# Kernel optimization log

Hardware: AMD Instinct MI355X
Metric: run time of the kernel (lower is better)

## Reference

```python
import jax, jax.numpy as jnp
import numpy as np

B, T, C, H = 4, 2048, 1024, 16
D = C // H  # head_dim = 64


def setup_inputs() -> dict:
    key = jax.random.key(0)
    k1, k2, k3, k4, k5 = jax.random.split(key, 5)
    x = jax.random.normal(k1, (B, T, C), dtype=jnp.float32)
    # torch nn.Linear weights: [out_features, in_features]
    s = 1.0 / np.sqrt(C)
    qkv_w = jax.random.uniform(k2, (3 * C, C), dtype=jnp.float32, minval=-s, maxval=s)
    qkv_b = jax.random.uniform(k3, (3 * C,), dtype=jnp.float32, minval=-s, maxval=s)
    out_w = jax.random.uniform(k4, (C, C), dtype=jnp.float32, minval=-s, maxval=s)
    out_b = jax.random.uniform(k5, (C,), dtype=jnp.float32, minval=-s, maxval=s)
    # causal mask broadcastable to [B,H,T,T]; 0 (False) marks masked positions
    attn_mask = jnp.tril(jnp.ones((T, T), dtype=bool))[None, None]
    return {"x": x, "qkv_w": qkv_w, "qkv_b": qkv_b, "out_w": out_w,
            "out_b": out_b, "attn_mask": attn_mask}


def reference(x, qkv_w, qkv_b, out_w, out_b, attn_mask):
    qkv = x @ qkv_w.T + qkv_b                      # [B,T,3C]
    q, k, v = jnp.split(qkv, 3, axis=-1)
    # [B,T,C] -> [B,H,T,D]
    q = q.reshape(B, T, H, D).transpose(0, 2, 1, 3)
    k = k.reshape(B, T, H, D).transpose(0, 2, 1, 3)
    v = v.reshape(B, T, H, D).transpose(0, 2, 1, 3)
    scale = 1.0 / np.sqrt(D)
    attn = jnp.einsum('bhqd,bhkd->bhqk', q, k) * scale   # [B,H,T,T]
    neg = jnp.finfo(attn.dtype).min
    attn = jnp.where(attn_mask, attn, neg)
    attn = jax.nn.softmax(attn, axis=-1)
    out = jnp.einsum('bhqk,bhkd->bhqd', attn, v)          # [B,H,T,D]
    out = out.transpose(0, 2, 1, 3).reshape(B, T, C)
    return out @ out_w.T + out_b
```

## Files before the change

kernel.cpp:

```cpp
#include <hip/hip_runtime.h>
#include <hip/hip_bf16.h>

#define B_ 4
#define T_ 2048
#define C_ 1024
#define H_ 16
#define D_ 64

typedef __hip_bfloat16 bf16;
typedef float f32x4 __attribute__((ext_vector_type(4)));
typedef short bf16s8 __attribute__((ext_vector_type(8)));

#define NEG_BIG (-1e30f)

__device__ inline unsigned short f2bf(float f) {
  __hip_bfloat16 h = __float2bfloat16(f);
  return *reinterpret_cast<unsigned short*>(&h);
}
__device__ inline float bf_lo(unsigned u) {
  union { unsigned u; float f; } c; c.u = u << 16; return c.f;
}

__device__ inline void async_load16(const void* g, void* l) {
  __builtin_amdgcn_global_load_lds(
      (const __attribute__((address_space(1))) unsigned int*)g,
      (__attribute__((address_space(3))) unsigned int*)l, 16, 0, 0);
}

__device__ inline void plswap32(unsigned& a, unsigned& b) {
  auto r = __builtin_amdgcn_permlane32_swap(a, b, false, false);
  a = r[0]; b = r[1];
}
__device__ inline void plswap16(unsigned& a, unsigned& b) {
  auto r = __builtin_amdgcn_permlane16_swap(a, b, false, false);
  a = r[0]; b = r[1];
}

union U4 { uint4 u; unsigned short s[8]; };

__device__ inline uint4 load8(const void* base, size_t idx, int f32) {
  if (f32) {
    const float* p = (const float*)base + idx;
    float4 a = *(const float4*)p;
    float4 b = *(const float4*)(p + 4);
    U4 r;
    r.s[0] = f2bf(a.x); r.s[1] = f2bf(a.y); r.s[2] = f2bf(a.z); r.s[3] = f2bf(a.w);
    r.s[4] = f2bf(b.x); r.s[5] = f2bf(b.y); r.s[6] = f2bf(b.z); r.s[7] = f2bf(b.w);
    return r.u;
  }
  return *(const uint4*)((const unsigned short*)base + idx);
}

__global__ void detect_k(const unsigned short* __restrict__ w, int* __restrict__ flag) {
  int lane = threadIdx.x;
  bool big = false;
  for (int i = lane; i < 512; i += 64) {
    float f = bf_lo((unsigned)w[i]);
    if (!(fabsf(f) <= 1.0f)) big = true;
  }
  int any = __any(big);
  if (lane == 0) *flag = any ? 1 : 0;
}

#define R_X   1048576
#define R_WQ  (R_X + 393216)
#define R_WO  (R_WQ + 131072)
#define R_BQ  (R_WO + 384)
#define R_BO  (R_BQ + 128)
__global__ __launch_bounds__(256) void convert_all_k(
    const void* __restrict__ x, const void* __restrict__ wq,
    const void* __restrict__ wo, const void* __restrict__ bq,
    const void* __restrict__ bo,
    bf16* __restrict__ xd, bf16* __restrict__ wqd, bf16* __restrict__ wod,
    bf16* __restrict__ bqd, bf16* __restrict__ bod,
    const int* __restrict__ flag) {
  const int f32 = *flag;
  long long g = (long long)blockIdx.x * 256 + threadIdx.x;
  if (g >= R_BO) return;
  const void* src; bf16* dst; long long base;
  if (g < R_X)       { src = x;  dst = xd;  base = 0; }
  else if (g < R_WQ) { src = wq; dst = wqd; base = R_X; }
  else if (g < R_WO) { src = wo; dst = wod; base = R_WQ; }
  else if (g < R_BQ) { src = bq; dst = bqd; base = R_WO; }
  else               { src = bo; dst = bod; base = R_BQ; }
  size_t i = (size_t)(g - base) * 8;
  *(uint4*)(dst + i) = load8(src, i, f32);
}

template <int KDIM, int MROWS>
__device__ inline void gemm_core(const bf16* __restrict__ A,
                                 const bf16* __restrict__ W,
                                 int tm, int tn, int wm, int wn,
                                 f32x4 acc[MROWS / 32][4], bf16* As, bf16* Bs) {
  const int tid  = threadIdx.x;
  const int lane = tid & 63;
  const int rl   = lane & 15;
  const int kq   = (lane >> 4) * 8;

  for (int k0 = 0; k0 < KDIM; k0 += 32) {
    __syncthreads();
#pragma unroll
    for (int j = 0; j < MROWS / 64; ++j) {
      int f    = j * 4096 + tid * 16;
      int row  = f >> 6;
      int colb = f & 63;
      async_load16((const char*)A + ((size_t)(tm + row) * KDIM + k0) * 2 + colb,
                   (char*)As + f);
    }
#pragma unroll
    for (int j = 0; j < 2; ++j) {
      int f    = j * 4096 + tid * 16;
      int row  = f >> 6;
      int colb = f & 63;
      async_load16((const char*)W + ((size_t)(tn + row) * KDIM + k0) * 2 + colb,
                   (char*)Bs + f);
    }
    __syncthreads();

    bf16s8 af[MROWS / 32], bw[4];
#pragma unroll
    for (int mt = 0; mt < MROWS / 32; ++mt)
      af[mt] = *(const bf16s8*)(As + (wm + mt * 16 + rl) * 32 + kq);
#pragma unroll
    for (int nt = 0; nt < 4; ++nt)
      bw[nt] = *(const bf16s8*)(Bs + (wn + nt * 16 + rl) * 32 + kq);

#pragma unroll
    for (int mt = 0; mt < MROWS / 32; ++mt)
#pragma unroll
      for (int nt = 0; nt < 4; ++nt)
        acc[mt][nt] = __builtin_amdgcn_mfma_f32_16x16x32_bf16(af[mt], bw[nt],
                                                              acc[mt][nt], 0, 0, 0);
  }
}

#define CSTRIDE 72
#define FSTRIDE 68

__global__ __launch_bounds__(256) void gemm_qkv_k(
    const bf16* __restrict__ X, const bf16* __restrict__ W,
    const bf16* __restrict__ bias,
    bf16* __restrict__ q, bf16* __restrict__ k, bf16* __restrict__ v) {
  __shared__ __align__(16) char smem[4 * 64 * CSTRIDE * 2];
  bf16* As = (bf16*)smem;
  bf16* Bs = (bf16*)(smem + 8192);
  const int tid = threadIdx.x;
  const int wave = tid >> 6, lane = tid & 63;
  const int tm = blockIdx.x * 128, tn = blockIdx.y * 128;
  const int wm = (wave >> 1) * 64, wn = (wave & 1) * 64;
  f32x4 acc[4][4];
#pragma unroll
  for (int i = 0; i < 4; ++i)
#pragma unroll
    for (int j = 0; j < 4; ++j) acc[i][j] = 0.0f;

  gemm_core<C_, 128>(X, W, tm, tn, wm, wn, acc, As, Bs);

  __syncthreads();
  bf16* Cs = (bf16*)smem + wave * 64 * CSTRIDE;

  const int rl = lane & 15, qd = lane >> 4;
  const int nbase = tn + wn;
  const int which = nbase >> 10;
  const int h = (nbase & 1023) >> 6;
  const float sc = which == 0 ? 0.125f : 1.0f;
  const int mbase = tm + wm;
  const int b = mbase >> 11, t0 = mbase & 2047;
  bf16* dst = which == 0 ? q : (which == 1 ? k : v);
  bf16* base = dst + (((size_t)(b * H_ + h)) * T_ + t0) * D_;

#pragma unroll
  for (int nt = 0; nt < 4; ++nt) {
    float bv = __bfloat162float(bias[nbase + nt * 16 + rl]);
#pragma unroll
    for (int mt = 0; mt < 4; ++mt)
#pragma unroll
      for (int r = 0; r < 4; ++r)
        Cs[(mt * 16 + qd * 4 + r) * CSTRIDE + nt * 16 + rl] =
            __float2bfloat16((acc[mt][nt][r] + bv) * sc);
  }
#pragma unroll
  for (int it = 0; it < 8; ++it) {
    int row = it * 8 + (lane >> 3);
    uint4 val = *(const uint4*)(Cs + row * CSTRIDE + (lane & 7) * 8);
    *(uint4*)(base + row * D_ + (lane & 7) * 8) = val;
  }
}

__global__ __launch_bounds__(256) void gemm_out_k(
    const bf16* __restrict__ O, const bf16* __restrict__ W,
    const bf16* __restrict__ bias, const int* __restrict__ flag,
    void* __restrict__ out) {
  __shared__ __align__(16) char smem[4 * 32 * FSTRIDE * 4];
  bf16* As = (bf16*)smem;
  bf16* Bs = (bf16*)(smem + 4096);
  const int f32 = *flag;
  const int tid = threadIdx.x;
  const int wave = tid >> 6, lane = tid & 63;
  const int tm = blockIdx.x * 64, tn = blockIdx.y * 128;
  const int wm = (wave >> 1) * 32, wn = (wave & 1) * 64;
  f32x4 acc[2][4];
#pragma unroll
  for (int i = 0; i < 2; ++i)
#pragma unroll
    for (int j = 0; j < 4; ++j) acc[i][j] = 0.0f;

  gemm_core<C_, 64>(O, W, tm, tn, wm, wn, acc, As, Bs);

  __syncthreads();
  const int rl = lane & 15, qd = lane >> 4;

  if (f32) {
    float* Cs = (float*)(smem + wave * 32 * FSTRIDE * 4);
#pragma unroll
    for (int nt = 0; nt < 4; ++nt) {
      float bv = __bfloat162float(bias[tn + wn + nt * 16 + rl]);
#pragma unroll
      for (int mt = 0; mt < 2; ++mt)
#pragma unroll
        for (int r = 0; r < 4; ++r)
          Cs[(mt * 16 + qd * 4 + r) * FSTRIDE + nt * 16 + rl] = acc[mt][nt][r] + bv;
    }
    float* obase = (float*)out + (size_t)(tm + wm) * C_ + tn + wn;
#pragma unroll
    for (int it = 0; it < 8; ++it) {
      int row = it * 4 + (lane >> 4);
      float4 val = *(const float4*)(Cs + row * FSTRIDE + (lane & 15) * 4);
      *(float4*)(obase + (size_t)row * C_ + (lane & 15) * 4) = val;
    }
  } else {
    bf16* Cs = (bf16*)(smem + wave * 32 * FSTRIDE * 4);
#pragma unroll
    for (int nt = 0; nt < 4; ++nt) {
      float bv = __bfloat162float(bias[tn + wn + nt * 16 + rl]);
#pragma unroll
      for (int mt = 0; mt < 2; ++mt)
#pragma unroll
        for (int r = 0; r < 4; ++r)
          Cs[(mt * 16 + qd * 4 + r) * CSTRIDE + nt * 16 + rl] =
              __float2bfloat16(acc[mt][nt][r] + bv);
    }
    bf16* obase = (bf16*)out + (size_t)(tm + wm) * C_ + tn + wn;
#pragma unroll
    for (int it = 0; it < 4; ++it) {
      int row = it * 8 + (lane >> 3);
      uint4 val = *(const uint4*)(Cs + row * CSTRIDE + (lane & 7) * 8);
      *(uint4*)(obase + (size_t)row * C_ + (lane & 7) * 8) = val;
    }
  }
}

__global__ __launch_bounds__(256) void fattn_k(
    const bf16* __restrict__ q, const bf16* __restrict__ k,
    const bf16* __restrict__ v, bf16* __restrict__ o) {
  __shared__ __align__(16) bf16 Ks[2][64 * 64];
  __shared__ __align__(16) bf16 Vs[2][64 * 64];
  const int tid = threadIdx.x, wave = tid >> 6, lane = tid & 63;
  const int rl = lane & 15, quad = lane >> 4;
  const int bh = blockIdx.x;
  const int b = bh >> 4, h = bh & 15;
  const size_t bhT = (size_t)bh * T_;
  const int sw0 = (quad ^ (rl & 7)) << 3;
  const int sw1 = ((quad | 4) ^ (rl & 7)) << 3;

  bf16s8 ones;
#pragma unroll
  for (int i = 0; i < 8; ++i) ones[i] = (short)0x3F80;

  const int qb = 31 - blockIdx.y;
  const int q0 = qb * 64;

  const int kr0 = tid >> 3;
  const int kc0 = ((tid & 7) ^ (kr0 & 7)) << 4;
  const char* kstage = (const char*)k + (bhT + kr0) * (D_ * 2) + kc0;

  const int kp = tid & 31, dg = tid >> 5;
  const bf16* vstage = v + (bhT + 2 * kp) * D_ + dg * 8;

  const bf16* qr = q + (bhT + q0 + wave * 16 + rl) * D_;
  bf16s8 qf0 = *(const bf16s8*)(qr + quad * 8);
  bf16s8 qf1 = *(const bf16s8*)(qr + 32 + quad * 8);

  f32x4 oacc[4], lacc;
#pragma unroll
  for (int nt = 0; nt < 4; ++nt) oacc[nt] = 0.0f;
  lacc = 0.0f;

  const int nchunk = qb + 1;

  {
    async_load16(kstage, (char*)Ks[0] + tid * 16);
    async_load16(kstage + 32 * 128, (char*)Ks[0] + 4096 + tid * 16);
    uint4 va = *(const uint4*)(vstage);
    uint4 vb = *(const uint4*)(vstage + D_);
    const unsigned* au = (const unsigned*)&va;
    const unsigned* bu = (const unsigned*)&vb;
#pragma unroll
    for (int m = 0; m < 4; ++m) {
      unsigned lo = (au[m] & 0xffffu) | (bu[m] << 16);
      unsigned hi = (au[m] >> 16) | (bu[m] & 0xffff0000u);
      int d0 = dg * 8 + 2 * m;
      int o0 = d0 * 64 + (((kp >> 2) ^ (2 * m)) << 3) + 2 * (kp & 3);
      int o1 = (d0 + 1) * 64 + (((kp >> 2) ^ (2 * m + 1)) << 3) + 2 * (kp & 3);
      *(unsigned*)(Vs[0] + o0) = lo;
      *(unsigned*)(Vs[0] + o1) = hi;
    }
  }
  __syncthreads();

  int cur = 0;
#pragma unroll 1
  for (int c = 0; c < nchunk; ++c) {
    const bf16* Kc = Ks[cur];
    const bf16* Vc = Vs[cur];
    const bool pf = (c + 1 < nchunk);

    uint4 va, vb;
    if (pf) {
      const char* ks = kstage + (size_t)(c + 1) * 8192;
      char* kd = (char*)Ks[cur ^ 1] + tid * 16;
      async_load16(ks, kd);
      async_load16(ks + 32 * 128, kd + 4096);
      const bf16* vs = vstage + (size_t)(c + 1) * 4096;
      va = *(const uint4*)(vs);
      vb = *(const uint4*)(vs + D_);
    }

    const int t0 = q0 + wave * 16;
    const int k0 = c << 6;

    f32x4 s[4];
#pragma unroll
    for (int nt = 0; nt < 4; ++nt) s[nt] = 0.0f;
#pragma unroll
    for (int nt = 0; nt < 4; ++nt) {
      int key = nt * 16 + rl;
      bf16s8 kb0 = *(const bf16s8*)(Kc + key * 64 + sw0);
      bf16s8 kb1 = *(const bf16s8*)(Kc + key * 64 + sw1);
      s[nt] = __builtin_amdgcn_mfma_f32_16x16x32_bf16(kb0, qf0, s[nt], 0, 0, 0);
      s[nt] = __builtin_amdgcn_mfma_f32_16x16x32_bf16(kb1, qf1, s[nt], 0, 0, 0);
    }

    if (c == nchunk - 1) {
      int t = t0 + rl;
#pragma unroll
      for (int nt = 0; nt < 4; ++nt)
#pragma unroll
        for (int r = 0; r < 4; ++r) {
          int key = k0 + nt * 16 + quad * 4 + r;
          if (key > t) s[nt][r] = NEG_BIG;
        }
    }

    unsigned pk[4][2];
#pragma unroll
    for (int nt = 0; nt < 4; ++nt) {
#pragma unroll
      for (int r = 0; r < 4; ++r)
        s[nt][r] = __expf(fminf(s[nt][r], 30.0f));
      pk[nt][0] = (unsigned)f2bf(s[nt][0]) | ((unsigned)f2bf(s[nt][1]) << 16);
      pk[nt][1] = (unsigned)f2bf(s[nt][2]) | ((unsigned)f2bf(s[nt][3]) << 16);
    }

    union { unsigned w[4]; bf16s8 v; } u0, u1;
    {
      unsigned a = pk[0][0], bq_ = pk[1][0];
      plswap32(a, bq_); plswap16(a, bq_);
      u0.w[0] = a; u0.w[2] = bq_;
      a = pk[0][1]; bq_ = pk[1][1];
      plswap32(a, bq_); plswap16(a, bq_);
      u0.w[1] = a; u0.w[3] = bq_;
      a = pk[2][0]; bq_ = pk[3][0];
      plswap32(a, bq_); plswap16(a, bq_);
      u1.w[0] = a; u1.w[2] = bq_;
      a = pk[2][1]; bq_ = pk[3][1];
      plswap32(a, bq_); plswap16(a, bq_);
      u1.w[1] = a; u1.w[3] = bq_;
    }
    bf16s8 pa0 = u0.v, pa1 = u1.v;

    lacc = __builtin_amdgcn_mfma_f32_16x16x32_bf16(pa0, ones, lacc, 0, 0, 0);
    lacc = __builtin_amdgcn_mfma_f32_16x16x32_bf16(pa1, ones, lacc, 0, 0, 0);
#pragma unroll
    for (int nt = 0; nt < 4; ++nt) {
      int d = nt * 16 + rl;
      bf16s8 vb0 = *(const bf16s8*)(Vc + d * 64 + sw0);
      bf16s8 vb1 = *(const bf16s8*)(Vc + d * 64 + sw1);
      oacc[nt] = __builtin_amdgcn_mfma_f32_16x16x32_bf16(pa0, vb0, oacc[nt], 0, 0, 0);
      oacc[nt] = __builtin_amdgcn_mfma_f32_16x16x32_bf16(pa1, vb1, oacc[nt], 0, 0, 0);
    }

    if (pf) {
      bf16* Vn = Vs[cur ^ 1];
      const unsigned* au = (const unsigned*)&va;
      const unsigned* bu = (const unsigned*)&vb;
#pragma unroll
      for (int m = 0; m < 4; ++m) {
        unsigned lo = (au[m] & 0xffffu) | (bu[m] << 16);
        unsigned hi = (au[m] >> 16) | (bu[m] & 0xffff0000u);
        int d0 = dg * 8 + 2 * m;
        int o0 = d0 * 64 + (((kp >> 2) ^ (2 * m)) << 3) + 2 * (kp & 3);
        int o1 = (d0 + 1) * 64 + (((kp >> 2) ^ (2 * m + 1)) << 3) + 2 * (kp & 3);
        *(unsigned*)(Vn + o0) = lo;
        *(unsigned*)(Vn + o1) = hi;
      }
    }
    __syncthreads();
    cur ^= 1;
  }

  f32x4 linv;
#pragma unroll
  for (int r = 0; r < 4; ++r) linv[r] = 1.0f / lacc[r];
#pragma unroll
  for (int nt = 0; nt < 4; ++nt) {
    int d = nt * 16 + rl;
#pragma unroll
    for (int r = 0; r < 4; ++r) {
      int t = q0 + wave * 16 + quad * 4 + r;
      o[((size_t)b * T_ + t) * C_ + h * D_ + d] =
          __float2bfloat16(oacc[nt][r] * linv[r]);
    }
  }
}

extern "C" void kernel_launch(void* const* d_in, const int* in_sizes, int n_in,
                              void* d_out, int out_size, void* d_ws, size_t ws_size,
                              hipStream_t stream) {
  (void)in_sizes; (void)n_in; (void)out_size; (void)ws_size;
  const void* x     = d_in[0];
  const void* qkv_w = d_in[1];
  const void* qkv_b = d_in[2];
  const void* out_w = d_in[3];
  const void* out_b = d_in[4];

  const size_t nqkv = (size_t)B_ * T_ * C_;
  char* ws = (char*)d_ws;
  int*  flag = (int*)ws;
  bf16* q   = (bf16*)(ws + 256);
  bf16* kk  = q + nqkv;
  bf16* vv  = kk + nqkv;
  bf16* oo  = vv + nqkv;
  bf16* xbf = oo;
  bf16* wqkv = oo + nqkv;
  bf16* wout = wqkv + 3 * C_ * C_;
  bf16* bqkv = wout + C_ * C_;
  bf16* bout = bqkv + 3 * C_;

  detect_k<<<1, 64, 0, stream>>>((const unsigned short*)qkv_w, flag);
  convert_all_k<<<(R_BO + 255) / 256, 256, 0, stream>>>(
      x, qkv_w, out_w, qkv_b, out_b, xbf, wqkv, wout, bqkv, bout, flag);

  gemm_qkv_k<<<dim3(64, 24), 256, 0, stream>>>(xbf, wqkv, bqkv, q, kk, vv);
  fattn_k<<<dim3(64, 32), 256, 0, stream>>>(q, kk, vv, oo);
  gemm_out_k<<<dim3(128, 8), 256, 0, stream>>>(oo, wout, bout, flag, d_out);
}
```

Measured before the change: 271.7 us.

## Double query tile per attention block to reuse K/V tiles across two row groups

Each attention block now processes 128 query rows (two 16-row groups per wave) instead of 64, so every K/V tile staged in shared memory feeds twice as many MFMAs, and the grid is halved. Query-block order is remapped with a small permutation to mix heavy and light causal blocks. Waves skip fully masked chunks. The cost is more registers per wave, fewer blocks, and possible idle waves within a block on diagonal chunks.

```diff
diff --git a/kernel.cpp b/kernel.cpp
--- a/kernel.cpp
+++ b/kernel.cpp
@@ -34,6 +34,16 @@
 __device__ inline void plswap16(unsigned& a, unsigned& b) {
   auto r = __builtin_amdgcn_permlane16_swap(a, b, false, false);
   a = r[0]; b = r[1];
+}
+
+__device__ inline void pk_to_frags(const unsigned pk[4][2], bf16s8& p0, bf16s8& p1) {
+  union { unsigned w[4]; bf16s8 v; } u0, u1;
+  unsigned a, b2;
+  a = pk[0][0]; b2 = pk[1][0]; plswap32(a, b2); plswap16(a, b2); u0.w[0] = a; u0.w[2] = b2;
+  a = pk[0][1]; b2 = pk[1][1]; plswap32(a, b2); plswap16(a, b2); u0.w[1] = a; u0.w[3] = b2;
+  a = pk[2][0]; b2 = pk[3][0]; plswap32(a, b2); plswap16(a, b2); u1.w[0] = a; u1.w[2] = b2;
+  a = pk[2][1]; b2 = pk[3][1]; plswap32(a, b2); plswap16(a, b2); u1.w[1] = a; u1.w[3] = b2;
+  p0 = u0.v; p1 = u1.v;
 }
 
 union U4 { uint4 u; unsigned short s[8]; };
@@ -267,8 +277,9 @@
 #pragma unroll
   for (int i = 0; i < 8; ++i) ones[i] = (short)0x3F80;
 
-  const int qb = 31 - blockIdx.y;
-  const int q0 = qb * 64;
+  const int y = blockIdx.y;
+  const int qbb = (y & 12) | (((y & 3) + (y >> 2)) & 3);
+  const int q0 = qbb * 128;
 
   const int kr0 = tid >> 3;
   const int kc0 = ((tid & 7) ^ (kr0 & 7)) << 4;
@@ -277,16 +288,20 @@
   const int kp = tid & 31, dg = tid >> 5;
   const bf16* vstage = v + (bhT + 2 * kp) * D_ + dg * 8;
 
-  const bf16* qr = q + (bhT + q0 + wave * 16 + rl) * D_;
-  bf16s8 qf0 = *(const bf16s8*)(qr + quad * 8);
-  bf16s8 qf1 = *(const bf16s8*)(qr + 32 + quad * 8);
-
-  f32x4 oacc[4], lacc;
-#pragma unroll
-  for (int nt = 0; nt < 4; ++nt) oacc[nt] = 0.0f;
-  lacc = 0.0f;
-
-  const int nchunk = qb + 1;
+  const int t0a = q0 + wave * 32;
+  const int t0b = t0a + 16;
+  const bf16* qra = q + (bhT + t0a + rl) * D_;
+  bf16s8 qf0a = *(const bf16s8*)(qra + quad * 8);
+  bf16s8 qf1a = *(const bf16s8*)(qra + 32 + quad * 8);
+  bf16s8 qf0b = *(const bf16s8*)(qra + 16 * D_ + quad * 8);
+  bf16s8 qf1b = *(const bf16s8*)(qra + 16 * D_ + 32 + quad * 8);
+
+  f32x4 oaccA[4], oaccB[4], laccA, laccB;
+#pragma unroll
+  for (int nt = 0; nt < 4; ++nt) { oaccA[nt] = 0.0f; oaccB[nt] = 0.0f; }
+  laccA = 0.0f; laccB = 0.0f;
+
+  const int nchunk = 2 * qbb + 2;
 
   {
     async_load16(kstage, (char*)Ks[0] + tid * 16);
@@ -326,68 +341,77 @@
       vb = *(const uint4*)(vs + D_);
     }
 
-    const int t0 = q0 + wave * 16;
     const int k0 = c << 6;
 
-    f32x4 s[4];
-#pragma unroll
-    for (int nt = 0; nt < 4; ++nt) s[nt] = 0.0f;
-#pragma unroll
-    for (int nt = 0; nt < 4; ++nt) {
-      int key = nt * 16 + rl;
-      bf16s8 kb0 = *(const bf16s8*)(Kc + key * 64 + sw0);
-      bf16s8 kb1 = *(const bf16s8*)(Kc + key * 64 + sw1);
-      s[nt] = __builtin_amdgcn_mfma_f32_16x16x32_bf16(kb0, qf0, s[nt], 0, 0, 0);
-      s[nt] = __builtin_amdgcn_mfma_f32_16x16x32_bf16(kb1, qf1, s[nt], 0, 0, 0);
-    }
-
-    if (c == nchunk - 1) {
-      int t = t0 + rl;
-#pragma unroll
-      for (int nt = 0; nt < 4; ++nt)
+    if (k0 <= t0a + 15) {
+      f32x4 sA[4], sB[4];
+#pragma unroll
+      for (int nt = 0; nt < 4; ++nt) { sA[nt] = 0.0f; sB[nt] = 0.0f; }
+#pragma unroll
+      for (int nt = 0; nt < 4; ++nt) {
+        int key = nt * 16 + rl;
+        bf16s8 kb0 = *(const bf16s8*)(Kc + key * 64 + sw0);
+        bf16s8 kb1 = *(const bf16s8*)(Kc + key * 64 + sw1);
+        sA[nt] = __builtin_amdgcn_mfma_f32_16x16x32_bf16(kb0, qf0a, sA[nt], 0, 0, 0);
+        sA[nt] = __builtin_amdgcn_mfma_f32_16x16x32_bf16(kb1, qf1a, sA[nt], 0, 0, 0);
+        sB[nt] = __builtin_amdgcn_mfma_f32_16x16x32_bf16(kb0, qf0b, sB[nt], 0, 0, 0);
+        sB[nt] = __builtin_amdgcn_mfma_f32_16x16x32_bf16(kb1, qf1b, sB[nt], 0, 0, 0);
+      }
+
+      if (k0 + 63 > t0a) {
+        int t = t0a + rl;
+#pragma unroll
+        for (int nt = 0; nt < 4; ++nt)
+#pragma unroll
+          for (int r = 0; r < 4; ++r) {
+            int key = k0 + nt * 16 + quad * 4 + r;
+            if (key > t) sA[nt][r] = NEG_BIG;
+          }
+      }
+      if (k0 + 63 > t0b) {
+        int t = t0b + rl;
+#pragma unroll
+        for (int nt = 0; nt < 4; ++nt)
+#pragma unroll
+          for (int r = 0; r < 4; ++r) {
+            int key = k0 + nt * 16 + quad * 4 + r;
+            if (key > t) sB[nt][r] = NEG_BIG;
+          }
+      }
+
+      unsigned pkA[4][2], pkB[4][2];
+#pragma unroll
+      for (int nt = 0; nt < 4; ++nt) {
 #pragma unroll
         for (int r = 0; r < 4; ++r) {
-          int key = k0 + nt * 16 + quad * 4 + r;
-          if (key > t) s[nt][r] = NEG_BIG;
+          sA[nt][r] = __expf(fminf(sA[nt][r], 30.0f));
+          sB[nt][r] = __expf(fminf(sB[nt][r], 30.0f));
         }
-    }
-
-    unsigned pk[4][2];
-#pragma unroll
-    for (int nt = 0; nt < 4; ++nt) {
-#pragma unroll
-      for (int r = 0; r < 4; ++r)
-        s[nt][r] = __expf(fminf(s[nt][r], 30.0f));
-      pk[nt][0] = (unsigned)f2bf(s[nt][0]) | ((unsigned)f2bf(s[nt][1]) << 16);
-      pk[nt][1] = (unsigned)f2bf(s[nt][2]) | ((unsigned)f2bf(s[nt][3]) << 16);
-    }
-
-    union { unsigned w[4]; bf16s8 v; } u0, u1;
-    {
-      unsigned a = pk[0][0], bq_ = pk[1][0];
-      plswap32(a, bq_); plswap16(a, bq_);
-      u0.w[0] = a; u0.w[2] = bq_;
-      a = pk[0][1]; bq_ = pk[1][1];
-      plswap32(a, bq_); plswap16(a, bq_);
-      u0.w[1] = a; u0.w[3] = bq_;
-      a = pk[2][0]; bq_ = pk[3][0];
-      plswap32(a, bq_); plswap16(a, bq_);
-      u1.w[0] = a; u1.w[2] = bq_;
-      a = pk[2][1]; bq_ = pk[3][1];
-      plswap32(a, bq_); plswap16(a, bq_);
-      u1.w[1] = a; u1.w[3] = bq_;
-    }
-    bf16s8 pa0 = u0.v, pa1 = u1.v;
-
-    lacc = __builtin_amdgcn_mfma_f32_16x16x32_bf16(pa0, ones, lacc, 0, 0, 0);
-    lacc = __builtin_amdgcn_mfma_f32_16x16x32_bf16(pa1, ones, lacc, 0, 0, 0);
-#pragma unroll
-    for (int nt = 0; nt < 4; ++nt) {
-      int d = nt * 16 + rl;
-      bf16s8 vb0 = *(const bf16s8*)(Vc + d * 64 + sw0);
-      bf16s8 vb1 = *(const bf16s8*)(Vc + d * 64 + sw1);
-      oacc[nt] = __builtin_amdgcn_mfma_f32_16x16x32_bf16(pa0, vb0, oacc[nt], 0, 0, 0);
-      oacc[nt] = __builtin_amdgcn_mfma_f32_16x16x32_bf16(pa1, vb1, oacc[nt], 0, 0, 0);
+        pkA[nt][0] = (unsigned)f2bf(sA[nt][0]) | ((unsigned)f2bf(sA[nt][1]) << 16);
+        pkA[nt][1] = (unsigned)f2bf(sA[nt][2]) | ((unsigned)f2bf(sA[nt][3]) << 16);
+        pkB[nt][0] = (unsigned)f2bf(sB[nt][0]) | ((unsigned)f2bf(sB[nt][1]) << 16);
+        pkB[nt][1] = (unsigned)f2bf(sB[nt][2]) | ((unsigned)f2bf(sB[nt][3]) << 16);
+      }
+
+      bf16s8 paA0, paA1, paB0, paB1;
+      pk_to_frags(pkA, paA0, paA1);
+      pk_to_frags(pkB, paB0, paB1);
+
+      laccA = __builtin_amdgcn_mfma_f32_16x16x32_bf16(paA0, ones, laccA, 0, 0, 0);
+      laccA = __builtin_amdgcn_mfma_f32_16x16x32_bf16(paA1, ones, laccA, 0, 0, 0);
+      laccB = __builtin_amdgcn_mfma_f32_16x16x32_bf16(paB0, ones, laccB, 0, 0, 0);
+      laccB = __builtin_amdgcn_mfma_f32_16x16x32_bf16(paB1, ones, laccB, 0, 0, 0);
+
+#pragma unroll
+      for (int nt = 0; nt < 4; ++nt) {
+        int d = nt * 16 + rl;
+        bf16s8 vb0 = *(const bf16s8*)(Vc + d * 64 + sw0);
+        bf16s8 vb1 = *(const bf16s8*)(Vc + d * 64 + sw1);
+        oaccA[nt] = __builtin_amdgcn_mfma_f32_16x16x32_bf16(paA0, vb0, oaccA[nt], 0, 0, 0);
+        oaccA[nt] = __builtin_amdgcn_mfma_f32_16x16x32_bf16(paA1, vb1, oaccA[nt], 0, 0, 0);
+        oaccB[nt] = __builtin_amdgcn_mfma_f32_16x16x32_bf16(paB0, vb0, oaccB[nt], 0, 0, 0);
+        oaccB[nt] = __builtin_amdgcn_mfma_f32_16x16x32_bf16(paB1, vb1, oaccB[nt], 0, 0, 0);
+      }
     }
 
     if (pf) {
@@ -409,17 +433,23 @@
     cur ^= 1;
   }
 
-  f32x4 linv;
-#pragma unroll
-  for (int r = 0; r < 4; ++r) linv[r] = 1.0f / lacc[r];
+  f32x4 linvA, linvB;
+#pragma unroll
+  for (int r = 0; r < 4; ++r) {
+    linvA[r] = 1.0f / laccA[r];
+    linvB[r] = 1.0f / laccB[r];
+  }
 #pragma unroll
   for (int nt = 0; nt < 4; ++nt) {
     int d = nt * 16 + rl;
 #pragma unroll
     for (int r = 0; r < 4; ++r) {
-      int t = q0 + wave * 16 + quad * 4 + r;
-      o[((size_t)b * T_ + t) * C_ + h * D_ + d] =
-          __float2bfloat16(oacc[nt][r] * linv[r]);
+      int tA = t0a + quad * 4 + r;
+      int tB = t0b + quad * 4 + r;
+      o[((size_t)b * T_ + tA) * C_ + h * D_ + d] =
+          __float2bfloat16(oaccA[nt][r] * linvA[r]);
+      o[((size_t)b * T_ + tB) * C_ + h * D_ + d] =
+          __float2bfloat16(oaccB[nt][r] * linvB[r]);
     }
   }
 }
@@ -452,6 +482,6 @@
       x, qkv_w, out_w, qkv_b, out_b, xbf, wqkv, wout, bqkv, bout, flag);
 
   gemm_qkv_k<<<dim3(64, 24), 256, 0, stream>>>(xbf, wqkv, bqkv, q, kk, vv);
-  fattn_k<<<dim3(64, 32), 256, 0, stream>>>(q, kk, vv, oo);
+  fattn_k<<<dim3(64, 16), 256, 0, stream>>>(q, kk, vv, oo);
   gemm_out_k<<<dim3(128, 8), 256, 0, stream>>>(oo, wout, bout, flag, d_out);
 }
```

New measurement: 286.5 us. +5.4%, slower.
